# Kernel optimization log

Hardware: AMD Instinct MI355X
Metric: run time of the kernel (lower is better)

## Reference

```python
import jax, jax.numpy as jnp
import numpy as np
from jax import lax

B, SEQ, PRED, CIN = 32, 336, 336, 7
ALL = SEQ + PRED
DM, DFF, NFFT, WIN, HOP = 64, 64, 64, 64, 8
NF = ALL // HOP + 1  # 85 STFT frames (center=True)
EL, CL, MARK = 2, 3, 4


def _conv2d(x, w, b, dil, pad):
    y = lax.conv_general_dilated(x, w, (1, 1), [(pad, pad), (pad, pad)],
                                 rhs_dilation=(dil, dil),
                                 dimension_numbers=('NCHW', 'OIHW', 'NCHW'))
    return y + b[None, :, None, None]


def _cconv(xr, xi, wr, wi, br, bi, dil, pad):
    # complex conv: (conv_r + i*conv_i)(xr + i*xi)
    rr = _conv2d(xr, wr, br, dil, pad)
    ii = _conv2d(xi, wi, bi, dil, pad)
    ri = _conv2d(xi, wr, br, dil, pad)
    ir = _conv2d(xr, wi, bi, dil, pad)
    return rr - ii, ri + ir


def _block(x, p):
    # x: [B, ALL, DM]; STFT per channel series (vectorized over B*DM, no python batch loop)
    xp = jnp.pad(x.transpose(0, 2, 1), ((0, 0), (0, 0), (NFFT // 2, NFFT // 2)), mode='reflect')
    idx = jnp.arange(NF)[:, None] * HOP + jnp.arange(NFFT)[None, :]
    win = 0.5 - 0.5 * jnp.cos(2.0 * jnp.pi * jnp.arange(WIN, dtype=jnp.float32) / WIN)  # periodic hann
    frames = xp[:, :, idx] * win  # [B, DM, NF, NFFT]
    S = jnp.fft.fft(frames, axis=-1) / jnp.sqrt(jnp.float32(NFFT))  # normalized=True (ortho)
    Sr = S.real.transpose(0, 1, 3, 2).astype(jnp.float32)  # [B, DM, NFFT, NF]
    Si = S.imag.transpose(0, 1, 3, 2).astype(jnp.float32)
    # complex 'qk' attention: compl_mul1d('ijxk,ijyk->ijxy', S, S)
    qk_r = jnp.einsum('bnxk,bnyk->bnxy', Sr, Sr) - jnp.einsum('bnxk,bnyk->bnxy', Si, Si)
    qk_i = jnp.einsum('bnxk,bnyk->bnxy', Sr, Si) + jnp.einsum('bnxk,bnyk->bnxy', Si, Sr)
    g_r = jax.nn.sigmoid(qk_r)
    g_i = jax.nn.sigmoid(qk_i)
    ar = jnp.einsum('bnxy,bnyz->bnxz', g_r, Sr) - jnp.einsum('bnxy,bnyz->bnxz', g_i, Si)
    ai = jnp.einsum('bnxy,bnyz->bnxz', g_r, Si) + jnp.einsum('bnxy,bnyz->bnxz', g_i, Sr)
    outs_r, outs_i = [], []
    yr, yi = _cconv(ar, ai, p['c0_wr'], p['c0_wi'], p['c0_br'], p['c0_bi'], 1, 0)
    outs_r.append(jax.nn.relu(yr)); outs_i.append(jax.nn.relu(yi))
    for k in range(1, CL):
        hr, hi = _cconv(ar, ai, p['cA_wr'][k - 1], p['cA_wi'][k - 1], p['cA_br'][k - 1], p['cA_bi'][k - 1], k, k)
        yr, yi = _cconv(hr, hi, p['cB_wr'][k - 1], p['cB_wi'][k - 1], p['cB_br'][k - 1], p['cB_bi'][k - 1], k, k)
        outs_r.append(jax.nn.relu(yr)); outs_i.append(jax.nn.relu(yi))
    mr = jnp.mean(jnp.stack(outs_r, -1), -1)
    mi = jnp.mean(jnp.stack(outs_i, -1), -1)
    y = mr * p['l0_w'][0, 0] + mi * p['l0_w'][0, 1] + p['l0_b'][0]  # Linear(2 -> 1) over (real, imag)
    y = y.mean(axis=2)  # mean over freq axis -> [B, DM, NF]
    y = jnp.einsum('bnf,af->bna', y, p['l2_w']) + p['l2_b']  # l2: NF -> ALL
    return y.transpose(0, 2, 1)  # [B, ALL, DM]


def _ln(x, g, b):
    m = x.mean(-1, keepdims=True)
    v = ((x - m) ** 2).mean(-1, keepdims=True)
    return (x - m) / jnp.sqrt(v + 1e-5) * g + b


def _forward(x_enc, x_mark_enc, tok_w, temp_w, pl_w, pl_b, ln_g, ln_b,
             c0_wr, c0_wi, c0_br, c0_bi, cA_wr, cA_wi, cA_br, cA_bi,
             cB_wr, cB_wi, cB_br, cB_bi, l0_w, l0_b, l2_w, l2_b,
             cv_w, cv_b, l1_w, l1_b, proj_w, proj_b):
    means = x_enc.mean(1, keepdims=True)
    xe = x_enc - means
    stdev = jnp.sqrt(xe.var(axis=1, keepdims=True) + 1e-5)
    xe = xe / stdev
    # DataEmbedding: circular token conv + sinusoidal PE + timeF linear (dropout=0)
    xv = jnp.pad(xe.transpose(0, 2, 1), ((0, 0), (0, 0), (1, 1)), mode='wrap')
    val = lax.conv_general_dilated(xv, tok_w, (1,), [(0, 0)],
                                   dimension_numbers=('NCH', 'OIH', 'NCH')).transpose(0, 2, 1)
    pos = jnp.arange(SEQ, dtype=jnp.float32)[:, None]
    div = jnp.exp(jnp.arange(0, DM, 2, dtype=jnp.float32) * (-np.log(10000.0) / DM))
    pe = jnp.zeros((SEQ, DM), jnp.float32).at[:, 0::2].set(jnp.sin(pos * div)).at[:, 1::2].set(jnp.cos(pos * div))
    enc = val + x_mark_enc @ temp_w.T + pe
    enc = jnp.einsum('btd,at->bad', enc, pl_w) + pl_b[None, :, None]  # predict_linear over time axis
    for l in range(EL):
        p = dict(c0_wr=c0_wr[l], c0_wi=c0_wi[l], c0_br=c0_br[l], c0_bi=c0_bi[l],
                 cA_wr=cA_wr[l], cA_wi=cA_wi[l], cA_br=cA_br[l], cA_bi=cA_bi[l],
                 cB_wr=cB_wr[l], cB_wi=cB_wi[l], cB_br=cB_br[l], cB_bi=cB_bi[l],
                 l0_w=l0_w[l], l0_b=l0_b[l], l2_w=l2_w[l], l2_b=l2_b[l])
        enc = _ln(_block(enc, p), ln_g, ln_b)
    # conv1d(in=ALL channels, kernel 3, stride 2, pad 1) over the d_model axis, then l1
    h = lax.conv_general_dilated(enc, cv_w, (2,), [(1, 1)],
                                 dimension_numbers=('NCH', 'OIH', 'NCH')) + cv_b[None, :, None]
    seq_series = (h @ l1_w.T)[..., 0] + l1_b[0]  # [B, ALL]
    dec = enc @ proj_w.T + proj_b
    dec = dec * stdev + means
    return dec[:, -PRED:, :], seq_series


def setup_inputs():
    key = jax.random.key(0)
    ks = jax.random.split(key, 24)
    def r(i, shape, s=0.02):
        return jax.random.normal(ks[i], shape, dtype=jnp.float32) * s
    return {
        'x_enc': jax.random.normal(ks[0], (B, SEQ, CIN), dtype=jnp.float32),
        'x_mark_enc': jax.random.normal(ks[1], (B, SEQ, MARK), dtype=jnp.float32),
        'x_dec': jax.random.normal(ks[2], (B, 48 + PRED, CIN), dtype=jnp.float32),
        'x_mark_dec': jax.random.normal(ks[3], (B, 48 + PRED, MARK), dtype=jnp.float32),
        'tok_w': r(4, (DM, CIN, 3), 0.1),
        'temp_w': r(5, (DM, MARK), 0.1),
        'pl_w': r(6, (ALL, SEQ), 0.05),
        'pl_b': jnp.zeros((ALL,), jnp.float32),
        'ln_g': jnp.ones((DM,), jnp.float32),
        'ln_b': jnp.zeros((DM,), jnp.float32),
        'c0_wr': r(7, (EL, DM, DM, 1, 1), 0.05),
        'c0_wi': r(8, (EL, DM, DM, 1, 1), 0.05),
        'c0_br': jnp.zeros((EL, DM), jnp.float32),
        'c0_bi': jnp.zeros((EL, DM), jnp.float32),
        'cA_wr': r(9, (EL, CL - 1, DFF, DM, 3, 3), 0.02),
        'cA_wi': r(10, (EL, CL - 1, DFF, DM, 3, 3), 0.02),
        'cA_br': jnp.zeros((EL, CL - 1, DFF), jnp.float32),
        'cA_bi': jnp.zeros((EL, CL - 1, DFF), jnp.float32),
        'cB_wr': r(11, (EL, CL - 1, DM, DFF, 3, 3), 0.02),
        'cB_wi': r(12, (EL, CL - 1, DM, DFF, 3, 3), 0.02),
        'cB_br': jnp.zeros((EL, CL - 1, DM), jnp.float32),
        'cB_bi': jnp.zeros((EL, CL - 1, DM), jnp.float32),
        'l0_w': r(13, (EL, 1, 2), 0.5),
        'l0_b': jnp.zeros((EL, 1), jnp.float32),
        'l2_w': r(14, (EL, ALL, NF), 0.05),
        'l2_b': jnp.zeros((EL, ALL), jnp.float32),
        'cv_w': r(15, (ALL, ALL, 3), 0.02),
        'cv_b': jnp.zeros((ALL,), jnp.float32),
        'l1_w': r(16, (1, DM // 2), 0.1),
        'l1_b': jnp.zeros((1,), jnp.float32),
        'proj_w': r(17, (CIN, DM), 0.1),
        'proj_b': jnp.zeros((CIN,), jnp.float32),
    }


def reference(x_enc, x_mark_enc, x_dec, x_mark_dec, tok_w, temp_w, pl_w, pl_b, ln_g, ln_b,
              c0_wr, c0_wi, c0_br, c0_bi, cA_wr, cA_wi, cA_br, cA_bi,
              cB_wr, cB_wi, cB_br, cB_bi, l0_w, l0_b, l2_w, l2_b,
              cv_w, cv_b, l1_w, l1_b, proj_w, proj_b):
    del x_dec, x_mark_dec  # unused in the forecast path
    return _forward(x_enc, x_mark_enc, tok_w, temp_w, pl_w, pl_b, ln_g, ln_b,
                    c0_wr, c0_wi, c0_br, c0_bi, cA_wr, cA_wi, cA_br, cA_bi,
                    cB_wr, cB_wi, cB_br, cB_bi, l0_w, l0_b, l2_w, l2_b,
                    cv_w, cv_b, l1_w, l1_b, proj_w, proj_b)
```

## Files before the change

### kernel.cpp

```cpp
#include <hip/hip_runtime.h>

typedef __attribute__((ext_vector_type(8))) short short8v;
typedef __attribute__((ext_vector_type(4))) float f32x4;
typedef __attribute__((ext_vector_type(16))) float f32x16;

static constexpr int Bt = 32;
static constexpr int SEQ = 336, PRED = 336, CIN = 7, ALLT = 672;
static constexpr int DM = 64, NFFT = 64, HOP = 8, NF = 85;
static constexpr int MARK = 4;
static constexpr float INV3 = 1.0f / 3.0f;

__device__ inline short f2bf(float v) {
    unsigned u = __float_as_uint(v);
    u += 0x7fffu + ((u >> 16) & 1u);
    return (short)(u >> 16);
}
__device__ inline float bf2f(short h) {
    return __uint_as_float(((unsigned)(unsigned short)h) << 16);
}
__device__ inline int pack2(float r, float i) {
    return ((int)(unsigned short)f2bf(r)) | (((int)(unsigned short)f2bf(i)) << 16);
}
__device__ inline void async16(const int* g, short* l) {
    __builtin_amdgcn_global_load_lds(
        (const __attribute__((address_space(1))) unsigned int*)g,
        (__attribute__((address_space(3))) unsigned int*)l, 16, 0, 0);
}

__global__ __launch_bounds__(64) void k_stats(const float* __restrict__ x,
                                              float* __restrict__ mean,
                                              float* __restrict__ stdv) {
    int bc = blockIdx.x;
    int b = bc / CIN, c = bc % CIN;
    int lane = threadIdx.x;
    float s = 0.f, s2 = 0.f;
    for (int t = lane; t < SEQ; t += 64) {
        float v = x[(b * SEQ + t) * CIN + c];
        s += v; s2 += v * v;
    }
    for (int m = 32; m >= 1; m >>= 1) { s += __shfl_xor(s, m); s2 += __shfl_xor(s2, m); }
    if (lane == 0) {
        float mu = s / SEQ;
        float var = s2 / SEQ - mu * mu;
        mean[bc] = mu;
        stdv[bc] = sqrtf(var + 1e-5f);
    }
}

__global__ __launch_bounds__(256) void k_embed(const float* __restrict__ x,
                                               const float* __restrict__ mark,
                                               const float* __restrict__ tok_w,
                                               const float* __restrict__ temp_w,
                                               const float* __restrict__ mean,
                                               const float* __restrict__ stdv,
                                               float* __restrict__ enc0) {
    int i = blockIdx.x * 256 + threadIdx.x;
    if (i >= Bt * SEQ * DM) return;
    int d = i & 63;
    int t = (i >> 6) % SEQ;
    int b = i / (SEQ * DM);
    float val = 0.f;
    for (int c = 0; c < CIN; ++c) {
        float mu = mean[b * CIN + c];
        float is = 1.f / stdv[b * CIN + c];
        for (int j = 0; j < 3; ++j) {
            int tt = t + j - 1;
            if (tt < 0) tt += SEQ;
            if (tt >= SEQ) tt -= SEQ;
            float xv = (x[(b * SEQ + tt) * CIN + c] - mu) * is;
            val += xv * tok_w[(d * CIN + c) * 3 + j];
        }
    }
    float mk = 0.f;
    for (int m = 0; m < MARK; ++m) mk += mark[(b * SEQ + t) * MARK + m] * temp_w[d * MARK + m];
    float div = expf(-(float)(d & ~1) * (9.210340371976184f / (float)DM));
    float arg = (float)t * div;
    float pe = (d & 1) ? cosf(arg) : sinf(arg);
    enc0[i] = val + mk + pe;
}

__global__ __launch_bounds__(256) void k_plin2(const float* __restrict__ enc0,
                                               const float* __restrict__ pl_w,
                                               const float* __restrict__ pl_b,
                                               float* __restrict__ enc) {
    __shared__ float Et[56 * 64];
    __shared__ float Wt[56 * 49];
    int blk = blockIdx.x;
    int b = blk / 14, at = blk % 14;
    int abase = at * 48;
    int tid = threadIdx.x;
    int a0 = (tid & 15) * 3;
    int d0 = (tid >> 4) * 4;
    float acc[3][4];
#pragma unroll
    for (int q = 0; q < 3; ++q)
#pragma unroll
        for (int r = 0; r < 4; ++r) acc[q][r] = 0.f;
    for (int tc = 0; tc < 6; ++tc) {
        if (tc) __syncthreads();
        for (int i = tid; i < 56 * 64; i += 256)
            Et[i] = enc0[((size_t)b * SEQ + tc * 56) * DM + i];
        for (int i = tid; i < 48 * 56; i += 256) {
            int r = i / 56, c = i - r * 56;
            Wt[c * 49 + r] = pl_w[(size_t)(abase + r) * SEQ + tc * 56 + c];
        }
        __syncthreads();
#pragma unroll 4
        for (int t = 0; t < 56; ++t) {
            float4 e = *(const float4*)&Et[t * 64 + d0];
            float w0 = Wt[t * 49 + a0];
            float w1 = Wt[t * 49 + a0 + 1];
            float w2 = Wt[t * 49 + a0 + 2];
            acc[0][0] += w0 * e.x; acc[0][1] += w0 * e.y;
            acc[0][2] += w0 * e.z; acc[0][3] += w0 * e.w;
            acc[1][0] += w1 * e.x; acc[1][1] += w1 * e.y;
            acc[1][2] += w1 * e.z; acc[1][3] += w1 * e.w;
            acc[2][0] += w2 * e.x; acc[2][1] += w2 * e.y;
            acc[2][2] += w2 * e.z; acc[2][3] += w2 * e.w;
        }
    }
#pragma unroll
    for (int q = 0; q < 3; ++q) {
        int a = abase + a0 + q;
        float bias = pl_b[a];
        float4 o = {acc[q][0] + bias, acc[q][1] + bias, acc[q][2] + bias, acc[q][3] + bias};
        *(float4*)&enc[((size_t)b * ALLT + a) * DM + d0] = o;
    }
}

__global__ __launch_bounds__(256) void k_stqka(const float* __restrict__ enc, int b0,
                                               int* __restrict__ Apk,
                                               int* __restrict__ Apl) {
    __shared__ __align__(16) short L[54272];
    constexpr int TCH = 0, TCL = 4608, TSH = 9216, TSL = 13824;
    constexpr int XWH = 18432, XWL = 25344;
    float* xp  = (float*)&L[32256];
    float* twc = (float*)&L[33728];
    float* tws = (float*)&L[33984];
    constexpr int SRH = 0, SIH = 6656, SRL = 13312, SIL = 19968;
    constexpr int STRH = 26624, STRL = 33536, STIH = 40448, STIL = 47360;
    constexpr int GRH = 0, GRL = 4608, GIH = 9216, GIL = 13824;

    int bn = blockIdx.x;
    int bl = bn >> 6, n = bn & 63;
    int bg = b0 + bl;
    int tid = threadIdx.x;
    int lane = tid & 63, w = tid >> 6;
    int l31 = lane & 31, kg = lane >> 5;

    for (int i = tid; i < ALLT + NFFT; i += 256) {
        int j = i - 32;
        if (j < 0) j = -j;
        if (j > ALLT - 1) j = 2 * (ALLT - 1) - j;
        xp[i] = enc[((size_t)bg * ALLT + j) * DM + n];
    }
    if (tid < 64) {
        float ang = (6.283185307179586f / 64.f) * (float)tid;
        twc[tid] = cosf(ang);
        tws[tid] = sinf(ang);
    }
    __syncthreads();
    for (int i = tid; i < 64 * 64; i += 256) {
        int k = i >> 6, tt = i & 63;
        int m = (k * tt) & 63;
        float c = twc[m], s = tws[m];
        short ch = f2bf(c); short cl = f2bf(c - bf2f(ch));
        short sh = f2bf(s); short sl = f2bf(s - bf2f(sh));
        int o = k * 72 + tt;
        L[TCH + o] = ch; L[TCL + o] = cl; L[TSH + o] = sh; L[TSL + o] = sl;
    }
    for (int i = tid; i < 96 * 64; i += 256) {
        int f = i >> 6, tt = i & 63;
        float v = 0.f;
        if (f < 85) v = xp[f * HOP + tt] * (0.5f - 0.5f * twc[tt]) * 0.125f;
        short vh = f2bf(v); short vl = f2bf(v - bf2f(vh));
        int o = f * 72 + tt;
        L[XWH + o] = vh; L[XWL + o] = vl;
    }
    __syncthreads();

    int kt = w & 1;
    int ftA = (w < 2) ? 0 : 2;
    f32x16 srA, siA, srB, siB;
#pragma unroll
    for (int r = 0; r < 16; ++r) { srA[r] = 0.f; siA[r] = 0.f; srB[r] = 0.f; siB[r] = 0.f; }
#pragma unroll
    for (int tts = 0; tts < 4; ++tts) {
        int ko = (kt * 32 + l31) * 72 + tts * 16 + kg * 8;
        short8v ach = *(const short8v*)&L[TCH + ko];
        short8v acl = *(const short8v*)&L[TCL + ko];
        short8v ash = *(const short8v*)&L[TSH + ko];
        short8v asl = *(const short8v*)&L[TSL + ko];
        {
            int bo = (ftA * 32 + l31) * 72 + tts * 16 + kg * 8;
            short8v bh = *(const short8v*)&L[XWH + bo];
            short8v bl_ = *(const short8v*)&L[XWL + bo];
            srA = __builtin_amdgcn_mfma_f32_32x32x16_bf16(ach, bh, srA, 0, 0, 0);
            srA = __builtin_amdgcn_mfma_f32_32x32x16_bf16(acl, bh, srA, 0, 0, 0);
            srA = __builtin_amdgcn_mfma_f32_32x32x16_bf16(ach, bl_, srA, 0, 0, 0);
            siA = __builtin_amdgcn_mfma_f32_32x32x16_bf16(ash, bh, siA, 0, 0, 0);
            siA = __builtin_amdgcn_mfma_f32_32x32x16_bf16(asl, bh, siA, 0, 0, 0);
            siA = __builtin_amdgcn_mfma_f32_32x32x16_bf16(ash, bl_, siA, 0, 0, 0);
        }
        if (w < 2) {
            int bo = (32 + l31) * 72 + tts * 16 + kg * 8;
            short8v bh = *(const short8v*)&L[XWH + bo];
            short8v bl_ = *(const short8v*)&L[XWL + bo];
            srB = __builtin_amdgcn_mfma_f32_32x32x16_bf16(ach, bh, srB, 0, 0, 0);
            srB = __builtin_amdgcn_mfma_f32_32x32x16_bf16(acl, bh, srB, 0, 0, 0);
            srB = __builtin_amdgcn_mfma_f32_32x32x16_bf16(ach, bl_, srB, 0, 0, 0);
            siB = __builtin_amdgcn_mfma_f32_32x32x16_bf16(ash, bh, siB, 0, 0, 0);
            siB = __builtin_amdgcn_mfma_f32_32x32x16_bf16(asl, bh, siB, 0, 0, 0);
            siB = __builtin_amdgcn_mfma_f32_32x32x16_bf16(ash, bl_, siB, 0, 0, 0);
        }
    }
    __syncthreads();

    {
        int fA = ftA * 32 + l31;
#pragma unroll
        for (int r = 0; r < 16; ++r) {
            int k = kt * 32 + (r & 3) + 8 * (r >> 2) + 4 * kg;
            float sv = srA[r], iv = -siA[r];
            short rh = f2bf(sv); short rl = f2bf(sv - bf2f(rh));
            short ih = f2bf(iv); short il = f2bf(iv - bf2f(ih));
            L[SRH + k * 104 + fA] = rh; L[SRL + k * 104 + fA] = rl;
            L[SIH + k * 104 + fA] = ih; L[SIL + k * 104 + fA] = il;
            L[STRH + fA * 72 + k] = rh; L[STRL + fA * 72 + k] = rl;
            L[STIH + fA * 72 + k] = ih; L[STIL + fA * 72 + k] = il;
        }
        if (w < 2) {
            int fB = 32 + l31;
#pragma unroll
            for (int r = 0; r < 16; ++r) {
                int k = kt * 32 + (r & 3) + 8 * (r >> 2) + 4 * kg;
                float sv = srB[r], iv = -siB[r];
                short rh = f2bf(sv); short rl = f2bf(sv - bf2f(rh));
                short ih = f2bf(iv); short il = f2bf(iv - bf2f(ih));
                L[SRH + k * 104 + fB] = rh; L[SRL + k * 104 + fB] = rl;
                L[SIH + k * 104 + fB] = ih; L[SIL + k * 104 + fB] = il;
                L[STRH + fB * 72 + k] = rh; L[STRL + fB * 72 + k] = rl;
                L[STIH + fB * 72 + k] = ih; L[STIL + fB * 72 + k] = il;
            }
        }
    }
    __syncthreads();

    int mh = w >> 1, nh = w & 1;
    f32x16 P, Q, R;
#pragma unroll
    for (int r = 0; r < 16; ++r) { P[r] = 0.f; Q[r] = 0.f; R[r] = 0.f; }
#pragma unroll
    for (int f0 = 0; f0 < 96; f0 += 16) {
        int ka = f0 + kg * 8;
        int ra = (mh * 32 + l31) * 104 + ka;
        int rb = (nh * 32 + l31) * 104 + ka;
        short8v a_rh = *(const short8v*)&L[SRH + ra];
        short8v a_rl = *(const short8v*)&L[SRL + ra];
        short8v a_ih = *(const short8v*)&L[SIH + ra];
        short8v a_il = *(const short8v*)&L[SIL + ra];
        short8v b_rh = *(const short8v*)&L[SRH + rb];
        short8v b_rl = *(const short8v*)&L[SRL + rb];
        short8v b_ih = *(const short8v*)&L[SIH + rb];
        short8v b_il = *(const short8v*)&L[SIL + rb];
        P = __builtin_amdgcn_mfma_f32_32x32x16_bf16(a_rh, b_rh, P, 0, 0, 0);
        P = __builtin_amdgcn_mfma_f32_32x32x16_bf16(a_rl, b_rh, P, 0, 0, 0);
        P = __builtin_amdgcn_mfma_f32_32x32x16_bf16(a_rh, b_rl, P, 0, 0, 0);
        Q = __builtin_amdgcn_mfma_f32_32x32x16_bf16(a_ih, b_ih, Q, 0, 0, 0);
        Q = __builtin_amdgcn_mfma_f32_32x32x16_bf16(a_il, b_ih, Q, 0, 0, 0);
        Q = __builtin_amdgcn_mfma_f32_32x32x16_bf16(a_ih, b_il, Q, 0, 0, 0);
        R = __builtin_amdgcn_mfma_f32_32x32x16_bf16(a_rh, b_ih, R, 0, 0, 0);
        R = __builtin_amdgcn_mfma_f32_32x32x16_bf16(a_rl, b_ih, R, 0, 0, 0);
        R = __builtin_amdgcn_mfma_f32_32x32x16_bf16(a_rh, b_il, R, 0, 0, 0);
        R = __builtin_amdgcn_mfma_f32_32x32x16_bf16(a_ih, b_rh, R, 0, 0, 0);
        R = __builtin_amdgcn_mfma_f32_32x32x16_bf16(a_il, b_rh, R, 0, 0, 0);
        R = __builtin_amdgcn_mfma_f32_32x32x16_bf16(a_ih, b_rl, R, 0, 0, 0);
    }
    __syncthreads();

    {
        int y = nh * 32 + l31;
#pragma unroll
        for (int r = 0; r < 16; ++r) {
            int x = mh * 32 + (r & 3) + 8 * (r >> 2) + 4 * kg;
            float gr = 1.f / (1.f + __expf(-(P[r] - Q[r])));
            float gi = 1.f / (1.f + __expf(-R[r]));
            short gh = f2bf(gr); short gl = f2bf(gr - bf2f(gh));
            short jh = f2bf(gi); short jl = f2bf(gi - bf2f(jh));
            L[GRH + x * 72 + y] = gh; L[GRL + x * 72 + y] = gl;
            L[GIH + x * 72 + y] = jh; L[GIL + x * 72 + y] = jl;
        }
    }
    __syncthreads();

    int mg = w >> 1;
    int mtA = (mg == 0) ? 0 : 2;
    f32x16 u1A, u2A, u3A, u1B, u2B, u3B;
#pragma unroll
    for (int r = 0; r < 16; ++r) {
        u1A[r] = 0.f; u2A[r] = 0.f; u3A[r] = 0.f;
        u1B[r] = 0.f; u2B[r] = 0.f; u3B[r] = 0.f;
    }
#pragma unroll
    for (int y0 = 0; y0 < 64; y0 += 16) {
        int kb = y0 + kg * 8;
        int gb = (nh * 32 + l31) * 72 + kb;
        short8v bgrh = *(const short8v*)&L[GRH + gb];
        short8v bgrl = *(const short8v*)&L[GRL + gb];
        short8v bgih = *(const short8v*)&L[GIH + gb];
        short8v bgil = *(const short8v*)&L[GIL + gb];
        {
            int sa = (mtA * 32 + l31) * 72 + kb;
            short8v arh = *(const short8v*)&L[STRH + sa];
            short8v arl = *(const short8v*)&L[STRL + sa];
            short8v aih = *(const short8v*)&L[STIH + sa];
            short8v ail = *(const short8v*)&L[STIL + sa];
            u1A = __builtin_amdgcn_mfma_f32_32x32x16_bf16(arh, bgrh, u1A, 0, 0, 0);
            u1A = __builtin_amdgcn_mfma_f32_32x32x16_bf16(arl, bgrh, u1A, 0, 0, 0);
            u1A = __builtin_amdgcn_mfma_f32_32x32x16_bf16(arh, bgrl, u1A, 0, 0, 0);
            u2A = __builtin_amdgcn_mfma_f32_32x32x16_bf16(aih, bgih, u2A, 0, 0, 0);
            u2A = __builtin_amdgcn_mfma_f32_32x32x16_bf16(ail, bgih, u2A, 0, 0, 0);
            u2A = __builtin_amdgcn_mfma_f32_32x32x16_bf16(aih, bgil, u2A, 0, 0, 0);
            u3A = __builtin_amdgcn_mfma_f32_32x32x16_bf16(aih, bgrh, u3A, 0, 0, 0);
            u3A = __builtin_amdgcn_mfma_f32_32x32x16_bf16(ail, bgrh, u3A, 0, 0, 0);
            u3A = __builtin_amdgcn_mfma_f32_32x32x16_bf16(aih, bgrl, u3A, 0, 0, 0);
            u3A = __builtin_amdgcn_mfma_f32_32x32x16_bf16(arh, bgih, u3A, 0, 0, 0);
            u3A = __builtin_amdgcn_mfma_f32_32x32x16_bf16(arl, bgih, u3A, 0, 0, 0);
            u3A = __builtin_amdgcn_mfma_f32_32x32x16_bf16(arh, bgil, u3A, 0, 0, 0);
        }
        if (mg == 0) {
            int sa = (1 * 32 + l31) * 72 + kb;
            short8v arh = *(const short8v*)&L[STRH + sa];
            short8v arl = *(const short8v*)&L[STRL + sa];
            short8v aih = *(const short8v*)&L[STIH + sa];
            short8v ail = *(const short8v*)&L[STIL + sa];
            u1B = __builtin_amdgcn_mfma_f32_32x32x16_bf16(arh, bgrh, u1B, 0, 0, 0);
            u1B = __builtin_amdgcn_mfma_f32_32x32x16_bf16(arl, bgrh, u1B, 0, 0, 0);
            u1B = __builtin_amdgcn_mfma_f32_32x32x16_bf16(arh, bgrl, u1B, 0, 0, 0);
            u2B = __builtin_amdgcn_mfma_f32_32x32x16_bf16(aih, bgih, u2B, 0, 0, 0);
            u2B = __builtin_amdgcn_mfma_f32_32x32x16_bf16(ail, bgih, u2B, 0, 0, 0);
            u2B = __builtin_amdgcn_mfma_f32_32x32x16_bf16(aih, bgil, u2B, 0, 0, 0);
            u3B = __builtin_amdgcn_mfma_f32_32x32x16_bf16(aih, bgrh, u3B, 0, 0, 0);
            u3B = __builtin_amdgcn_mfma_f32_32x32x16_bf16(ail, bgrh, u3B, 0, 0, 0);
            u3B = __builtin_amdgcn_mfma_f32_32x32x16_bf16(aih, bgrl, u3B, 0, 0, 0);
            u3B = __builtin_amdgcn_mfma_f32_32x32x16_bf16(arh, bgih, u3B, 0, 0, 0);
            u3B = __builtin_amdgcn_mfma_f32_32x32x16_bf16(arl, bgih, u3B, 0, 0, 0);
            u3B = __builtin_amdgcn_mfma_f32_32x32x16_bf16(arh, bgil, u3B, 0, 0, 0);
        }
    }
    {
        size_t pkbase = ((size_t)(bl * 16 + (n >> 2)) * 64) * 85 * 4 + (n & 3);
        int x2 = nh * 32 + l31;
#pragma unroll
        for (int r = 0; r < 16; ++r) {
            int z = mtA * 32 + (r & 3) + 8 * (r >> 2) + 4 * kg;
            if (z < 85) {
                float ar = u1A[r] - u2A[r];
                float ai = u3A[r];
                size_t o = pkbase + ((size_t)x2 * 85 + z) * 4;
                short arh = f2bf(ar); short aih = f2bf(ai);
                Apk[o] = ((int)(unsigned short)arh) | (((int)(unsigned short)aih) << 16);
                Apl[o] = pack2(ar - bf2f(arh), ai - bf2f(aih));
            }
        }
        if (mg == 0) {
#pragma unroll
            for (int r = 0; r < 16; ++r) {
                int z = 32 + (r & 3) + 8 * (r >> 2) + 4 * kg;
                float ar = u1B[r] - u2B[r];
                float ai = u3B[r];
                size_t o = pkbase + ((size_t)x2 * 85 + z) * 4;
                short arh = f2bf(ar); short aih = f2bf(ai);
                Apk[o] = ((int)(unsigned short)arh) | (((int)(unsigned short)aih) << 16);
                Apl[o] = pack2(ar - bf2f(arh), ai - bf2f(aih));
            }
        }
    }
}

__global__ __launch_bounds__(256) void k_wprep(const float* __restrict__ cA_wr,
                                               const float* __restrict__ cA_wi,
                                               const float* __restrict__ cB_wr,
                                               const float* __restrict__ cB_wi,
                                               const float* __restrict__ c0_wr,
                                               const float* __restrict__ c0_wi,
                                               short* __restrict__ wt) {
    int idx = blockIdx.x * 256 + threadIdx.x;
    if (idx >= 1245184) return;
    int c32 = idx & 31;
    int m = (idx >> 5) & 127;
    int ci_l = c32 >> 1;
    int part = c32 & 1;
    int co = m & 63;
    const float *wr, *wi;
    size_t woff;
    bool lo = false;
    int chunk;
    if (idx < 1179648) {
        chunk = (idx >> 12) & 3;
        int tap = (idx >> 14) % 9;
        int conv = idx / 147456;
        int l = conv >> 2, k1 = (conv >> 1) & 1, ab = conv & 1;
        int ci = chunk * 16 + ci_l;
        woff = (((size_t)(l * 2 + k1) * 64 + co) * 64 + ci) * 9 + tap;
        wr = ab ? cB_wr : cA_wr;
        wi = ab ? cB_wi : cA_wi;
    } else {
        int i2 = idx - 1179648;
        chunk = (i2 >> 12) & 3;
        lo = (i2 >> 14) & 1;
        int l = i2 >> 15;
        int ci = chunk * 16 + ci_l;
        woff = ((size_t)(l * 64 + co)) * 64 + ci;
        wr = c0_wr; wi = c0_wi;
    }
    float a = wr[woff], bb = wi[woff];
    float v = (m < 64) ? (part ? -bb : a) : (part ? a : bb);
    if (lo) v = v - bf2f(f2bf(v));
    wt[idx] = f2bf(v);
}

__global__ __launch_bounds__(256, 4) void k_conv3p(const int* __restrict__ in_pk,
                                                   const short* __restrict__ wt,
                                                   const float* __restrict__ b_r,
                                                   const float* __restrict__ b_i,
                                                   int K, int mode,
                                                   const float* __restrict__ l0w,
                                                   int* __restrict__ out_pk,
                                                   float* __restrict__ yfull) {
    __shared__ __align__(16) short inT[2][1020 * 8];
    int blk = blockIdx.x;
    int swz = (blk & 7) * (gridDim.x >> 3) + (blk >> 3);
    int b = swz >> 6, x0 = swz & 63;
    int tid = threadIdx.x;
    int lane = tid & 63, wid = tid >> 6;
    int wrow = wid & 1, wcol = wid >> 1;
    int l15 = lane & 15, g = lane >> 4;

#define STAGE(CC, BUFI)                                                       \
    do {                                                                      \
        _Pragma("unroll")                                                     \
        for (int it = 0; it < 4; ++it) {                                      \
            int idx = tid + it * 256;                                         \
            if (idx < 1020) {                                                 \
                int f = idx % 85;                                             \
                int rc = idx / 85;                                            \
                int xr = rc >> 2, cg = rc & 3;                                \
                int xg = x0 + (xr - 1) * K;                                   \
                if ((unsigned)xg < 64u) {                                     \
                    const int* src = in_pk +                                  \
                        (((size_t)((b * 16 + (CC) * 4 + cg) * 64 + xg)) * 85 + f) * 4; \
                    async16(src, &inT[BUFI][(wid * 64 + it * 256) * 8]);      \
                }                                                             \
            }                                                                 \
        }                                                                     \
    } while (0)

    { int* p = (int*)&inT[0][0];
      for (int i = tid; i < 2 * 1020 * 4; i += 256) p[i] = 0; }
    __syncthreads();

    f32x4 acc[4][3];
#pragma unroll
    for (int a = 0; a < 4; ++a)
#pragma unroll
        for (int j = 0; j < 3; ++j) acc[a][j] = f32x4{0.f, 0.f, 0.f, 0.f};

    STAGE(0, 0);
    __syncthreads();

    int cur = 0;
    for (int chunk = 0; chunk < 4; ++chunk) {
        if (chunk == 0) STAGE(1, 1);
        else if (chunk == 1) STAGE(2, 0);
        else if (chunk == 2) STAGE(3, 1);
        const short* bb = &inT[cur][0];
#pragma unroll
        for (int u = 0; u < 3; ++u) {
#pragma unroll
            for (int v = 0; v < 3; ++v) {
                int tap = u * 3 + v;
                short8v afr[4];
#pragma unroll
                for (int a = 0; a < 4; ++a) {
                    int tile = (a < 2) ? (wrow * 2 + a) : (wrow * 2 + a + 2);
                    const short* ap = wt + ((((size_t)tap * 4 + chunk) * 8 + tile) * 16 + l15) * 32 + g * 8;
                    afr[a] = *(const short8v*)ap;
                }
                short8v bfr[3];
#pragma unroll
                for (int j = 0; j < 3; ++j) {
                    int fs = (wcol * 3 + j) * 16 + l15 + (v - 1) * K;
                    bool inr = ((unsigned)fs < 85u);
                    int fsc = inr ? fs : 0;
                    short8v t8 = *(const short8v*)&bb[((u * 4 + g) * 85 + fsc) * 8];
                    bfr[j] = inr ? t8 : short8v{0, 0, 0, 0, 0, 0, 0, 0};
                }
#pragma unroll
                for (int a = 0; a < 4; ++a)
#pragma unroll
                    for (int j = 0; j < 3; ++j)
                        acc[a][j] = __builtin_amdgcn_mfma_f32_16x16x32_bf16(afr[a], bfr[j],
                                                                            acc[a][j], 0, 0, 0);
            }
        }
        __syncthreads();
        cur ^= 1;
    }
#undef STAGE

    float w0 = 0.f, w1 = 0.f;
    if (mode == 1) { w0 = l0w[0]; w1 = l0w[1]; }
#pragma unroll
    for (int a = 0; a < 2; ++a) {
#pragma unroll
        for (int j = 0; j < 3; ++j) {
            int f = (wcol * 3 + j) * 16 + l15;
            if (f < NF) {
                if (mode == 0) {
                    int4 o;
#pragma unroll
                    for (int reg = 0; reg < 4; ++reg) {
                        int co = (wrow * 2 + a) * 16 + g * 4 + reg;
                        float vrq = acc[a][j][reg]     + b_r[co] - b_i[co];
                        float viq = acc[a + 2][j][reg] + b_r[co] + b_i[co];
                        ((int*)&o)[reg] = pack2(vrq, viq);
                    }
                    int co4 = (wrow * 2 + a) * 4 + g;
                    ((int4*)out_pk)[((size_t)((b * 16 + co4) * 64 + x0)) * 85 + f] = o;
                } else {
#pragma unroll
                    for (int reg = 0; reg < 4; ++reg) {
                        int co = (wrow * 2 + a) * 16 + g * 4 + reg;
                        float vrq = acc[a][j][reg]     + b_r[co] - b_i[co];
                        float viq = acc[a + 2][j][reg] + b_r[co] + b_i[co];
                        size_t o = ((size_t)(b * 64 + co) * 64 + x0) * NF + f;
                        yfull[o] += (fmaxf(vrq, 0.f) * w0 + fmaxf(viq, 0.f) * w1) * INV3;
                    }
                }
            }
        }
    }
}

__global__ __launch_bounds__(256, 4) void k_c0m(const int* __restrict__ Apk,
                                                const int* __restrict__ Apl,
                                                const short* __restrict__ wt,
                                                const float* __restrict__ b_r,
                                                const float* __restrict__ b_i,
                                                const float* __restrict__ l0w,
                                                float* __restrict__ yfull) {
    __shared__ __align__(16) short inT[100 * 80];
    int blk = blockIdx.x;
    int swz = (blk & 7) * (gridDim.x >> 3) + (blk >> 3);
    int b = swz >> 6, x0 = swz & 63;
    int tid = threadIdx.x;
    int lane = tid & 63, wid = tid >> 6;
    int wrow = wid & 1, wcol = wid >> 1;
    int l15 = lane & 15, g = lane >> 4;

    f32x4 acc[4][3];
#pragma unroll
    for (int a = 0; a < 4; ++a)
#pragma unroll
        for (int j = 0; j < 3; ++j) acc[a][j] = f32x4{0.f, 0.f, 0.f, 0.f};

    for (int chunk = 0; chunk < 4; ++chunk) {
        if (chunk > 0) __syncthreads();
        for (int idx = tid; idx < 340; idx += 256) {
            int f = idx % 85;
            int cg = idx / 85;
            size_t s4 = ((size_t)((b * 16 + chunk * 4 + cg) * 64 + x0)) * 85 + f;
            int4 dh = ((const int4*)Apk)[s4];
            int4 dl = ((const int4*)Apl)[s4];
            short* rowp = &inT[(f + 2) * 80];
            *(int4*)&rowp[cg * 8] = dh;
            *(int4*)&rowp[32 + cg * 8] = dl;
        }
        __syncthreads();
#pragma unroll
        for (int combo = 0; combo < 3; ++combo) {
            int wtap = (combo == 2) ? 1 : 0;
            int kkB = (combo == 1) ? 1 : 0;
            short8v afr[4];
#pragma unroll
            for (int a = 0; a < 4; ++a) {
                int tile = (a < 2) ? (wrow * 2 + a) : (wrow * 2 + a + 2);
                const short* ap = wt + ((((size_t)wtap * 4 + chunk) * 8 + tile) * 16 + l15) * 32 + g * 8;
                afr[a] = *(const short8v*)ap;
            }
            short8v bfr[3];
#pragma unroll
            for (int j = 0; j < 3; ++j) {
                int fs = (wcol * 3 + j) * 16 + l15 + 2;
                bfr[j] = *(const short8v*)&inT[fs * 80 + kkB * 32 + g * 8];
            }
#pragma unroll
            for (int a = 0; a < 4; ++a)
#pragma unroll
                for (int j = 0; j < 3; ++j)
                    acc[a][j] = __builtin_amdgcn_mfma_f32_16x16x32_bf16(afr[a], bfr[j],
                                                                        acc[a][j], 0, 0, 0);
        }
    }

    float w0 = l0w[0], w1 = l0w[1];
#pragma unroll
    for (int a = 0; a < 2; ++a) {
#pragma unroll
        for (int j = 0; j < 3; ++j) {
            int f = (wcol * 3 + j) * 16 + l15;
            if (f < NF) {
#pragma unroll
                for (int reg = 0; reg < 4; ++reg) {
                    int co = (wrow * 2 + a) * 16 + g * 4 + reg;
                    float vrq = acc[a][j][reg]     + b_r[co] - b_i[co];
                    float viq = acc[a + 2][j][reg] + b_r[co] + b_i[co];
                    size_t o = ((size_t)(b * 64 + co) * 64 + x0) * NF + f;
                    yfull[o] = (fmaxf(vrq, 0.f) * w0 + fmaxf(viq, 0.f) * w1) * INV3;
                }
            }
        }
    }
}

__global__ __launch_bounds__(256) void k_reduce2(const float* __restrict__ yfull,
                                                 const float* __restrict__ l0b,
                                                 float* __restrict__ y2) {
    __shared__ float fs[3][85];
    int bn = blockIdx.x;
    int tid = threadIdx.x;
    const float* p = yfull + (size_t)bn * 64 * 85;
    if (tid < 255) {
        int f = tid % 85, g = tid / 85;
        float s = 0.f;
        for (int x = g; x < 64; x += 3) s += p[x * 85 + f];
        fs[g][f] = s;
    }
    __syncthreads();
    if (tid < 85)
        y2[(size_t)bn * 85 + tid] = (fs[0][tid] + fs[1][tid] + fs[2][tid]) * (1.f / 64.f) + l0b[0];
}

__global__ __launch_bounds__(64) void k_l2ln(const float* __restrict__ y2,
                                             const float* __restrict__ l2w,
                                             const float* __restrict__ l2b,
                                             const float* __restrict__ g,
                                             const float* __restrict__ be,
                                             float* __restrict__ enc, int b0) {
    int bl = blockIdx.x / ALLT;
    int a = blockIdx.x % ALLT;
    int d = threadIdx.x;
    const float* wp = l2w + (size_t)a * NF;
    const float* yp = y2 + (size_t)(bl * 64 + d) * NF;
    float acc = l2b[a];
    for (int f = 0; f < NF; ++f) acc += yp[f] * wp[f];
    float s = acc, s2 = acc * acc;
    for (int m = 32; m >= 1; m >>= 1) { s += __shfl_xor(s, m); s2 += __shfl_xor(s2, m); }
    float mu = s * (1.f / 64.f);
    float var = s2 * (1.f / 64.f) - mu * mu;
    float rs = rsqrtf(var + 1e-5f);
    enc[((size_t)(b0 + bl) * ALLT + a) * DM + d] = (acc - mu) * rs * g[d] + be[d];
}

__global__ __launch_bounds__(256) void k_T(const float* __restrict__ enc,
                                           const float* __restrict__ l1w,
                                           float* __restrict__ T) {
    int i = blockIdx.x * 256 + threadIdx.x;
    if (i >= Bt * ALLT * 3) return;
    int j = i % 3;
    int rest = i / 3;
    int ci = rest % ALLT;
    int b = rest / ALLT;
    const float* e = enc + ((size_t)b * ALLT + ci) * DM;
    float s = 0.f;
    for (int hx = 0; hx < 32; ++hx) {
        int p = 2 * hx + j - 1;
        if (p >= 0 && p < DM) s += e[p] * l1w[hx];
    }
    T[i] = s;
}

__global__ __launch_bounds__(256) void k_seq(const float* __restrict__ T,
                                             const float* __restrict__ cvw,
                                             const float* __restrict__ cvb,
                                             const float* __restrict__ l1w,
                                             const float* __restrict__ l1b,
                                             float* __restrict__ out) {
    int i = blockIdx.x * 256 + threadIdx.x;
    if (i >= Bt * ALLT) return;
    int co = i % ALLT;
    int b = i / ALLT;
    float sl1 = 0.f;
    for (int hx = 0; hx < 32; ++hx) sl1 += l1w[hx];
    const float* tp = T + (size_t)b * ALLT * 3;
    const float* wp = cvw + (size_t)co * ALLT * 3;
    float s = 0.f;
    for (int q = 0; q < ALLT * 3; ++q) s += tp[q] * wp[q];
    out[i] = s + cvb[co] * sl1 + l1b[0];
}

__global__ __launch_bounds__(256) void k_dec(const float* __restrict__ enc,
                                             const float* __restrict__ pw,
                                             const float* __restrict__ pb,
                                             const float* __restrict__ mean,
                                             const float* __restrict__ stdv,
                                             float* __restrict__ out) {
    int i = blockIdx.x * 256 + threadIdx.x;
    if (i >= Bt * PRED * CIN) return;
    int c = i % CIN;
    int rest = i / CIN;
    int tt = rest % PRED;
    int b = rest / PRED;
    const float* e = enc + ((size_t)b * ALLT + SEQ + tt) * DM;
    const float* w = pw + c * DM;
    float s = pb[c];
    for (int d = 0; d < DM; ++d) s += e[d] * w[d];
    out[i] = s * stdv[b * CIN + c] + mean[b * CIN + c];
}

extern "C" void kernel_launch(void* const* d_in, const int* in_sizes, int n_in,
                              void* d_out, int out_size, void* d_ws, size_t ws_size,
                              hipStream_t stream) {
    (void)in_sizes; (void)n_in; (void)out_size;
    const float* x_enc  = (const float*)d_in[0];
    const float* x_mark = (const float*)d_in[1];
    const float* tok_w  = (const float*)d_in[4];
    const float* temp_w = (const float*)d_in[5];
    const float* pl_w   = (const float*)d_in[6];
    const float* pl_b   = (const float*)d_in[7];
    const float* ln_g   = (const float*)d_in[8];
    const float* ln_b   = (const float*)d_in[9];
    const float* c0_wr  = (const float*)d_in[10];
    const float* c0_wi  = (const float*)d_in[11];
    const float* c0_br  = (const float*)d_in[12];
    const float* c0_bi  = (const float*)d_in[13];
    const float* cA_wr  = (const float*)d_in[14];
    const float* cA_wi  = (const float*)d_in[15];
    const float* cA_br  = (const float*)d_in[16];
    const float* cA_bi  = (const float*)d_in[17];
    const float* cB_wr  = (const float*)d_in[18];
    const float* cB_wi  = (const float*)d_in[19];
    const float* cB_br  = (const float*)d_in[20];
    const float* cB_bi  = (const float*)d_in[21];
    const float* l0_w   = (const float*)d_in[22];
    const float* l0_b   = (const float*)d_in[23];
    const float* l2_w   = (const float*)d_in[24];
    const float* l2_b   = (const float*)d_in[25];
    const float* cv_w   = (const float*)d_in[26];
    const float* cv_b   = (const float*)d_in[27];
    const float* l1_w   = (const float*)d_in[28];
    const float* l1_b   = (const float*)d_in[29];
    const float* proj_w = (const float*)d_in[30];
    const float* proj_b = (const float*)d_in[31];

    float* out0 = (float*)d_out;
    float* out1 = out0 + (size_t)Bt * PRED * CIN;

    float* ws = (float*)d_ws;
    size_t off = 0;
    float* enc  = ws + off; off += (size_t)Bt * ALLT * DM;
    float* enc0 = ws + off; off += (size_t)Bt * SEQ * DM;
    float* mean = ws + off; off += 256;
    float* stdv = ws + off; off += 256;
    short* wtbuf = (short*)(ws + off); off += 622592;

    const size_t perb = (size_t)DM * NFFT * NF;
    int Bc = 32;
    while (Bc > 1) {
        size_t need = (off + (size_t)Bc * DM * NF + 4 * (size_t)Bc * perb) * sizeof(float);
        if (need <= ws_size) break;
        Bc >>= 1;
    }
    float* y2 = ws + off; off += (size_t)Bc * DM * NF;
    float* yfull = ws + off; off += (size_t)Bc * perb;
    int*   Apk = (int*)(ws + off); off += (size_t)Bc * perb;
    int*   Apl = (int*)(ws + off); off += (size_t)Bc * perb;
    int*   Hpk = (int*)(ws + off); off += (size_t)Bc * perb;
    float* Tb = enc0;

    k_stats<<<Bt * CIN, 64, 0, stream>>>(x_enc, mean, stdv);
    k_wprep<<<(1245184 + 255) / 256, 256, 0, stream>>>(cA_wr, cA_wi, cB_wr, cB_wi,
                                                       c0_wr, c0_wi, wtbuf);
    k_embed<<<(Bt * SEQ * DM + 255) / 256, 256, 0, stream>>>(x_enc, x_mark, tok_w, temp_w,
                                                             mean, stdv, enc0);
    k_plin2<<<Bt * 14, 256, 0, stream>>>(enc0, pl_w, pl_b, enc);

    for (int l = 0; l < 2; ++l) {
        for (int b0 = 0; b0 < Bt; b0 += Bc) {
            k_stqka<<<Bc * 64, 256, 0, stream>>>(enc, b0, Apk, Apl);
            k_c0m<<<Bc * 64, 256, 0, stream>>>(Apk, Apl, wtbuf + 1179648 + (size_t)l * 32768,
                                               c0_br + l * 64, c0_bi + l * 64,
                                               l0_w + l * 2, yfull);
            for (int k = 1; k <= 2; ++k) {
                int convA = l * 4 + (k - 1) * 2;
                size_t boff = ((size_t)l * 2 + (k - 1)) * 64;
                k_conv3p<<<Bc * 64, 256, 0, stream>>>(Apk, wtbuf + (size_t)convA * 147456,
                                                      cA_br + boff, cA_bi + boff, k, 0,
                                                      l0_w + l * 2, Hpk, yfull);
                k_conv3p<<<Bc * 64, 256, 0, stream>>>(Hpk, wtbuf + (size_t)(convA + 1) * 147456,
                                                      cB_br + boff, cB_bi + boff, k, 1,
                                                      l0_w + l * 2, Hpk, yfull);
            }
            k_reduce2<<<Bc * 64, 256, 0, stream>>>(yfull, l0_b + l, y2);
            k_l2ln<<<Bc * ALLT, 64, 0, stream>>>(y2, l2_w + (size_t)l * ALLT * NF,
                                                 l2_b + (size_t)l * ALLT, ln_g, ln_b, enc, b0);
        }
    }

    k_T<<<(Bt * ALLT * 3 + 255) / 256, 256, 0, stream>>>(enc, l1_w, Tb);
    k_seq<<<(Bt * ALLT + 255) / 256, 256, 0, stream>>>(Tb, cv_w, cv_b, l1_w, l1_b, out1);
    k_dec<<<(Bt * PRED * CIN + 255) / 256, 256, 0, stream>>>(enc, proj_w, proj_b, mean, stdv, out0);
}
```

Measured before the change: 1.474 ms.

## Drop low-order bf16 split of attention output and vectorize transposed LDS stores

The attention output A is no longer stored as a hi/lo bf16 pair. Only the single packed bf16 buffer is written, so the Apl buffer, its global writes, its loads in k_c0m and one of the three split-precision MFMA passes are removed. In k_stqka the transposed spectrum stores are grouped into 8-byte LDS writes, and the block index is swizzled so blocks are spread differently across the XCDs. This lowers memory traffic and MFMA work, but precision in the c0 conv input drops to plain bf16, which could hurt accuracy.

```diff
diff --git a/kernel.cpp b/kernel.cpp
--- a/kernel.cpp
+++ b/kernel.cpp
@@ -129,8 +129,7 @@
 }
 
 __global__ __launch_bounds__(256) void k_stqka(const float* __restrict__ enc, int b0,
-                                               int* __restrict__ Apk,
-                                               int* __restrict__ Apl) {
+                                               int* __restrict__ Apk) {
     __shared__ __align__(16) short L[54272];
     constexpr int TCH = 0, TCL = 4608, TSH = 9216, TSL = 13824;
     constexpr int XWH = 18432, XWL = 25344;
@@ -141,7 +140,8 @@
     constexpr int STRH = 26624, STRL = 33536, STIH = 40448, STIL = 47360;
     constexpr int GRH = 0, GRL = 4608, GIH = 9216, GIL = 13824;
 
-    int bn = blockIdx.x;
+    int blk = blockIdx.x;
+    int bn = (blk & 7) * (gridDim.x >> 3) + (blk >> 3);
     int bl = bn >> 6, n = bn & 63;
     int bg = b0 + bl;
     int tid = threadIdx.x;
@@ -219,28 +219,44 @@
     {
         int fA = ftA * 32 + l31;
 #pragma unroll
-        for (int r = 0; r < 16; ++r) {
-            int k = kt * 32 + (r & 3) + 8 * (r >> 2) + 4 * kg;
-            float sv = srA[r], iv = -siA[r];
-            short rh = f2bf(sv); short rl = f2bf(sv - bf2f(rh));
-            short ih = f2bf(iv); short il = f2bf(iv - bf2f(ih));
-            L[SRH + k * 104 + fA] = rh; L[SRL + k * 104 + fA] = rl;
-            L[SIH + k * 104 + fA] = ih; L[SIL + k * 104 + fA] = il;
-            L[STRH + fA * 72 + k] = rh; L[STRL + fA * 72 + k] = rl;
-            L[STIH + fA * 72 + k] = ih; L[STIL + fA * 72 + k] = il;
+        for (int rg = 0; rg < 4; ++rg) {
+            int k0 = kt * 32 + 8 * rg + 4 * kg;
+            short prh[4], prl[4], pih[4], pil[4];
+#pragma unroll
+            for (int q = 0; q < 4; ++q) {
+                int r = rg * 4 + q;
+                float sv = srA[r], iv = -siA[r];
+                short rh = f2bf(sv); short rl = f2bf(sv - bf2f(rh));
+                short ih = f2bf(iv); short il = f2bf(iv - bf2f(ih));
+                prh[q] = rh; prl[q] = rl; pih[q] = ih; pil[q] = il;
+                L[SRH + (k0 + q) * 104 + fA] = rh; L[SRL + (k0 + q) * 104 + fA] = rl;
+                L[SIH + (k0 + q) * 104 + fA] = ih; L[SIL + (k0 + q) * 104 + fA] = il;
+            }
+            *(long long*)&L[STRH + fA * 72 + k0] = *(long long*)prh;
+            *(long long*)&L[STRL + fA * 72 + k0] = *(long long*)prl;
+            *(long long*)&L[STIH + fA * 72 + k0] = *(long long*)pih;
+            *(long long*)&L[STIL + fA * 72 + k0] = *(long long*)pil;
         }
         if (w < 2) {
             int fB = 32 + l31;
 #pragma unroll
-            for (int r = 0; r < 16; ++r) {
-                int k = kt * 32 + (r & 3) + 8 * (r >> 2) + 4 * kg;
-                float sv = srB[r], iv = -siB[r];
-                short rh = f2bf(sv); short rl = f2bf(sv - bf2f(rh));
-                short ih = f2bf(iv); short il = f2bf(iv - bf2f(ih));
-                L[SRH + k * 104 + fB] = rh; L[SRL + k * 104 + fB] = rl;
-                L[SIH + k * 104 + fB] = ih; L[SIL + k * 104 + fB] = il;
-                L[STRH + fB * 72 + k] = rh; L[STRL + fB * 72 + k] = rl;
-                L[STIH + fB * 72 + k] = ih; L[STIL + fB * 72 + k] = il;
+            for (int rg = 0; rg < 4; ++rg) {
+                int k0 = kt * 32 + 8 * rg + 4 * kg;
+                short prh[4], prl[4], pih[4], pil[4];
+#pragma unroll
+                for (int q = 0; q < 4; ++q) {
+                    int r = rg * 4 + q;
+                    float sv = srB[r], iv = -siB[r];
+                    short rh = f2bf(sv); short rl = f2bf(sv - bf2f(rh));
+                    short ih = f2bf(iv); short il = f2bf(iv - bf2f(ih));
+                    prh[q] = rh; prl[q] = rl; pih[q] = ih; pil[q] = il;
+                    L[SRH + (k0 + q) * 104 + fB] = rh; L[SRL + (k0 + q) * 104 + fB] = rl;
+                    L[SIH + (k0 + q) * 104 + fB] = ih; L[SIL + (k0 + q) * 104 + fB] = il;
+                }
+                *(long long*)&L[STRH + fB * 72 + k0] = *(long long*)prh;
+                *(long long*)&L[STRL + fB * 72 + k0] = *(long long*)prl;
+                *(long long*)&L[STIH + fB * 72 + k0] = *(long long*)pih;
+                *(long long*)&L[STIL + fB * 72 + k0] = *(long long*)pil;
             }
         }
     }
@@ -354,25 +370,14 @@
 #pragma unroll
         for (int r = 0; r < 16; ++r) {
             int z = mtA * 32 + (r & 3) + 8 * (r >> 2) + 4 * kg;
-            if (z < 85) {
-                float ar = u1A[r] - u2A[r];
-                float ai = u3A[r];
-                size_t o = pkbase + ((size_t)x2 * 85 + z) * 4;
-                short arh = f2bf(ar); short aih = f2bf(ai);
-                Apk[o] = ((int)(unsigned short)arh) | (((int)(unsigned short)aih) << 16);
-                Apl[o] = pack2(ar - bf2f(arh), ai - bf2f(aih));
-            }
+            if (z < 85)
+                Apk[pkbase + ((size_t)x2 * 85 + z) * 4] = pack2(u1A[r] - u2A[r], u3A[r]);
         }
         if (mg == 0) {
 #pragma unroll
             for (int r = 0; r < 16; ++r) {
                 int z = 32 + (r & 3) + 8 * (r >> 2) + 4 * kg;
-                float ar = u1B[r] - u2B[r];
-                float ai = u3B[r];
-                size_t o = pkbase + ((size_t)x2 * 85 + z) * 4;
-                short arh = f2bf(ar); short aih = f2bf(ai);
-                Apk[o] = ((int)(unsigned short)arh) | (((int)(unsigned short)aih) << 16);
-                Apl[o] = pack2(ar - bf2f(arh), ai - bf2f(aih));
+                Apk[pkbase + ((size_t)x2 * 85 + z) * 4] = pack2(u1B[r] - u2B[r], u3B[r]);
             }
         }
     }
@@ -544,13 +549,12 @@
 }
 
 __global__ __launch_bounds__(256, 4) void k_c0m(const int* __restrict__ Apk,
-                                                const int* __restrict__ Apl,
                                                 const short* __restrict__ wt,
                                                 const float* __restrict__ b_r,
                                                 const float* __restrict__ b_i,
                                                 const float* __restrict__ l0w,
                                                 float* __restrict__ yfull) {
-    __shared__ __align__(16) short inT[100 * 80];
+    __shared__ __align__(16) short inT[100 * 40];
     int blk = blockIdx.x;
     int swz = (blk & 7) * (gridDim.x >> 3) + (blk >> 3);
     int b = swz >> 6, x0 = swz & 63;
@@ -572,16 +576,11 @@
             int cg = idx / 85;
             size_t s4 = ((size_t)((b * 16 + chunk * 4 + cg) * 64 + x0)) * 85 + f;
             int4 dh = ((const int4*)Apk)[s4];
-            int4 dl = ((const int4*)Apl)[s4];
-            short* rowp = &inT[(f + 2) * 80];
-            *(int4*)&rowp[cg * 8] = dh;
-            *(int4*)&rowp[32 + cg * 8] = dl;
+            *(int4*)&inT[(f + 2) * 40 + cg * 8] = dh;
         }
         __syncthreads();
 #pragma unroll
-        for (int combo = 0; combo < 3; ++combo) {
-            int wtap = (combo == 2) ? 1 : 0;
-            int kkB = (combo == 1) ? 1 : 0;
+        for (int wtap = 0; wtap < 2; ++wtap) {
             short8v afr[4];
 #pragma unroll
             for (int a = 0; a < 4; ++a) {
@@ -593,7 +592,7 @@
 #pragma unroll
             for (int j = 0; j < 3; ++j) {
                 int fs = (wcol * 3 + j) * 16 + l15 + 2;
-                bfr[j] = *(const short8v*)&inT[fs * 80 + kkB * 32 + g * 8];
+                bfr[j] = *(const short8v*)&inT[fs * 40 + g * 8];
             }
 #pragma unroll
             for (int a = 0; a < 4; ++a)
@@ -768,14 +767,13 @@
     const size_t perb = (size_t)DM * NFFT * NF;
     int Bc = 32;
     while (Bc > 1) {
-        size_t need = (off + (size_t)Bc * DM * NF + 4 * (size_t)Bc * perb) * sizeof(float);
+        size_t need = (off + (size_t)Bc * DM * NF + 3 * (size_t)Bc * perb) * sizeof(float);
         if (need <= ws_size) break;
         Bc >>= 1;
     }
     float* y2 = ws + off; off += (size_t)Bc * DM * NF;
     float* yfull = ws + off; off += (size_t)Bc * perb;
     int*   Apk = (int*)(ws + off); off += (size_t)Bc * perb;
-    int*   Apl = (int*)(ws + off); off += (size_t)Bc * perb;
     int*   Hpk = (int*)(ws + off); off += (size_t)Bc * perb;
     float* Tb = enc0;
 
@@ -788,8 +786,8 @@
 
     for (int l = 0; l < 2; ++l) {
         for (int b0 = 0; b0 < Bt; b0 += Bc) {
-            k_stqka<<<Bc * 64, 256, 0, stream>>>(enc, b0, Apk, Apl);
-            k_c0m<<<Bc * 64, 256, 0, stream>>>(Apk, Apl, wtbuf + 1179648 + (size_t)l * 32768,
+            k_stqka<<<Bc * 64, 256, 0, stream>>>(enc, b0, Apk);
+            k_c0m<<<Bc * 64, 256, 0, stream>>>(Apk, wtbuf + 1179648 + (size_t)l * 32768,
                                                c0_br + l * 64, c0_bi + l * 64,
                                                l0_w + l * 2, yfull);
             for (int k = 1; k <= 2; ++k) {
```

Result: faster. 1.369 ms (-7.1%).
